# Performance work log

Hardware: AMD Instinct MI355X
Metric: run time of the kernel (lower is better)

The kernel has to match this reference:

```python
import jax, jax.numpy as jnp
import numpy as np

N_HEAD = 16
ROPE_BASE = 10000.0


def _rope(x):
    # x: (B, T, H, D), interleaved even/odd (GPT-NeoX style)
    B, T, H, D = x.shape
    inv_freq = 1.0 / (ROPE_BASE ** (jnp.arange(0, D, 2, dtype=jnp.float32) / D))
    t = jnp.arange(T, dtype=jnp.float32)
    freqs = t[:, None] * inv_freq[None, :]            # (T, D//2)
    cos = jnp.cos(freqs)[None, :, None, :]            # (1, T, 1, D//2)
    sin = jnp.sin(freqs)[None, :, None, :]
    x1, x2 = x[..., ::2], x[..., 1::2]
    y1 = x1 * cos - x2 * sin
    y2 = x1 * sin + x2 * cos
    return jnp.stack((y1, y2), axis=-1).reshape(B, T, H, D)


def setup_inputs() -> dict:
    key = jax.random.key(0)
    k1, k2, k3 = jax.random.split(key, 3)
    B, T, C = 4, 2048, 1024
    x = jax.random.normal(k1, (B, T, C), dtype=jnp.float32)
    W_attn = jax.random.normal(k2, (C, 3 * C), dtype=jnp.float32) * (1.0 / np.sqrt(C))
    W_proj = jax.random.normal(k3, (C, C), dtype=jnp.float32) * (1.0 / np.sqrt(C))
    return {"x": x, "W_attn": W_attn, "W_proj": W_proj}


def reference(x, W_attn, W_proj):
    B, T, C = x.shape
    H = N_HEAD
    D = C // H
    qkv = jnp.einsum('btc,cf->btf', x, W_attn)        # (B, T, 3C)
    q, k, v = jnp.split(qkv, 3, axis=-1)
    q = _rope(q.reshape(B, T, H, D))
    k = _rope(k.reshape(B, T, H, D))
    v = v.reshape(B, T, H, D)
    # (B, H, T, D)
    q = q.transpose(0, 2, 1, 3)
    k = k.transpose(0, 2, 1, 3)
    v = v.transpose(0, 2, 1, 3)
    scale = 1.0 / np.sqrt(D).astype(np.float32)
    scores = jnp.einsum('bhqd,bhkd->bhqk', q, k) * scale
    causal = jnp.tril(jnp.ones((T, T), dtype=bool))
    scores = jnp.where(causal[None, None], scores, jnp.finfo(scores.dtype).min)
    att = jax.nn.softmax(scores, axis=-1)
    y = jnp.einsum('bhqk,bhkd->bhqd', att, v)         # (B, H, T, D)
    y = y.transpose(0, 2, 1, 3).reshape(B, T, C)
    return jnp.einsum('btc,cf->btf', y, W_proj)
```

## Files before the change

kernel.cpp:

```cpp
#include <hip/hip_runtime.h>
#include <hip/hip_bf16.h>
#include <math.h>

typedef __attribute__((ext_vector_type(8))) __bf16 bf16x8;
typedef __attribute__((ext_vector_type(4))) float f32x4;
typedef __attribute__((ext_vector_type(16))) float f32x16;
typedef __attribute__((ext_vector_type(4))) unsigned short us4;

#define DEVINL static __device__ __forceinline__

DEVINL unsigned short f2bf(float f) {
  union { float f; unsigned int u; } v; v.f = f;
  return (unsigned short)((v.u + 0x7FFFu + ((v.u >> 16) & 1u)) >> 16);
}

DEVINL unsigned short f2bf_hw(float f) {
  __bf16 h = (__bf16)f;
  union { __bf16 h; unsigned short u; } v; v.h = h;
  return v.u;
}

DEVINL unsigned pk2(float a, float b) {
  return (unsigned)f2bf_hw(a) | ((unsigned)f2bf_hw(b) << 16);
}

DEVINL f32x4 mfma16(bf16x8 a, bf16x8 b, f32x4 c) {
  return __builtin_amdgcn_mfma_f32_16x16x32_bf16(a, b, c, 0, 0, 0);
}
DEVINL f32x16 mfma32(bf16x8 a, bf16x8 b, f32x16 c) {
  return __builtin_amdgcn_mfma_f32_32x32x16_bf16(a, b, c, 0, 0, 0);
}

#define GLOAD16(GP, LP)                                                        \
  __builtin_amdgcn_global_load_lds(                                            \
      (const __attribute__((address_space(1))) void*)(GP),                     \
      (__attribute__((address_space(3))) void*)(LP), 16, 0, 0)

static constexpr int kB = 4, kT = 2048, kC = 1024, kH = 16, kD = 64;
static constexpr int kM = kB * kT;

__global__ void cvt_x_kernel(const float* __restrict__ x,
                             unsigned short* __restrict__ xb, int n4) {
  int stride = gridDim.x * blockDim.x;
  for (int i = blockIdx.x * blockDim.x + threadIdx.x; i < n4; i += stride) {
    float4 v = ((const float4*)x)[i];
    us4 o;
    o[0] = f2bf(v.x); o[1] = f2bf(v.y); o[2] = f2bf(v.z); o[3] = f2bf(v.w);
    ((us4*)xb)[i] = o;
  }
}

__global__ void transpose_w_kernel(const float* __restrict__ W,
                                   unsigned short* __restrict__ WT,
                                   int K, int N) {
  __shared__ float tile[32][33];
  int n0 = blockIdx.x * 32, k0 = blockIdx.y * 32;
  int tx = threadIdx.x, ty = threadIdx.y;
#pragma unroll
  for (int i = 0; i < 4; ++i)
    tile[ty + i * 8][tx] = W[(size_t)(k0 + ty + i * 8) * N + n0 + tx];
  __syncthreads();
#pragma unroll
  for (int i = 0; i < 4; ++i)
    WT[(size_t)(n0 + ty + i * 8) * K + k0 + tx] = f2bf(tile[tx][ty + i * 8]);
}

__global__ void rope_table_kernel(float* __restrict__ cosT,
                                  float* __restrict__ sinT) {
  int idx = blockIdx.x * blockDim.x + threadIdx.x;
  if (idx >= kT * 32) return;
  int d2 = idx >> 11, t = idx & 2047;
  double ang = (double)t * pow(10000.0, -(double)d2 / 32.0);
  cosT[idx] = (float)cos(ang);
  sinT[idx] = (float)sin(ang);
}

template <int EPI>
__global__ __launch_bounds__(256) void gemm_bt_kernel(
    const unsigned short* __restrict__ A, const unsigned short* __restrict__ Bt,
    float* __restrict__ Cout, int Ndim, int Kdim,
    const float* __restrict__ cosT, const float* __restrict__ sinT,
    unsigned short* __restrict__ Qr, unsigned short* __restrict__ Kr,
    unsigned short* __restrict__ Vtg) {
  __shared__ unsigned short As[3][128 * 32];
  __shared__ unsigned short Bs[3][128 * 32];
  const int tid = threadIdx.x;
  const int wave = tid >> 6, lane = tid & 63;

  const int nwg = gridDim.x * gridDim.y;
  const int lin = blockIdx.y * gridDim.x + blockIdx.x;
  const int wg = (lin & 7) * (nwg >> 3) + (lin >> 3);
  const int n0 = (wg % gridDim.x) * 128, m0 = (wg / gridDim.x) * 128;

  const int wr = wave >> 1, wc = wave & 1;

  f32x4 acc[4][4] = {};

  const int srow = lane >> 2;
  const int scol = (((lane & 3) ^ ((lane >> 3) & 3)) << 3);
  const int fr = lane & 15;
  const int kswz = (((lane >> 4) ^ ((lane >> 1) & 3)) << 3);

  auto stage = [&](int k0, int bb) {
#pragma unroll
    for (int o = 0; o < 2; ++o) {
      int s = o * 4 + wave;
      int row = s * 16 + srow;
      GLOAD16(A + (size_t)(m0 + row) * Kdim + k0 + scol, &As[bb][s * 512]);
      GLOAD16(Bt + (size_t)(n0 + row) * Kdim + k0 + scol, &Bs[bb][s * 512]);
    }
  };

  const int NT = Kdim >> 5;
  stage(0, 0);
  stage(32, 1);

  for (int t = 0; t < NT; ++t) {
    const int buf = t % 3;
    if (t + 1 < NT) {
      asm volatile("s_waitcnt vmcnt(4)" ::: "memory");
    } else {
      asm volatile("s_waitcnt vmcnt(0)" ::: "memory");
    }
    __builtin_amdgcn_sched_barrier(0);
    __builtin_amdgcn_s_barrier();
    if (t + 2 < NT) stage((t + 2) << 5, (t + 2) % 3);

    bf16x8 af[4], bfr[4];
#pragma unroll
    for (int f = 0; f < 4; ++f)
      af[f] = *(const bf16x8*)&As[buf][(wr * 64 + f * 16 + fr) * 32 + kswz];
#pragma unroll
    for (int f = 0; f < 4; ++f)
      bfr[f] = *(const bf16x8*)&Bs[buf][(wc * 64 + f * 16 + fr) * 32 + kswz];
#pragma unroll
    for (int i = 0; i < 4; ++i)
#pragma unroll
      for (int j = 0; j < 4; ++j)
        acc[i][j] = mfma16(af[i], bfr[j], acc[i][j]);

    asm volatile("s_waitcnt lgkmcnt(0)" ::: "memory");
    __builtin_amdgcn_sched_barrier(0);
  }

  const int lr = (lane >> 4) * 4;
  const int fc = lane & 15;
  if (EPI == 0) {
#pragma unroll
    for (int i = 0; i < 4; ++i) {
      int mb = m0 + wr * 64 + i * 16 + lr;
#pragma unroll
      for (int j = 0; j < 4; ++j) {
        int n = n0 + wc * 64 + j * 16 + fc;
#pragma unroll
        for (int r = 0; r < 4; ++r)
          Cout[(size_t)(mb + r) * Ndim + n] = acc[i][j][r];
      }
    }
  } else {
#pragma unroll
    for (int i = 0; i < 4; ++i) {
      int mb = m0 + wr * 64 + i * 16 + lr;
      int b = mb >> 11, t0 = mb & 2047;
#pragma unroll
      for (int j = 0; j < 4; ++j) {
        int n = n0 + wc * 64 + j * 16 + fc;
        int sec = n >> 10;
        int c = n & 1023;
        int h = c >> 6, d = c & 63;
        size_t bh = (size_t)(b * 16 + h);
        if (sec == 2) {
          us4 pk;
#pragma unroll
          for (int r = 0; r < 4; ++r) pk[r] = f2bf(acc[i][j][r]);
          *(us4*)&Vtg[(bh * 64 + d) * 2048 + t0] = pk;
        } else {
          unsigned short* dst = (sec == 0) ? Qr : Kr;
          float4 c4 = *(const float4*)&cosT[(d >> 1) * 2048 + t0];
          float4 s4 = *(const float4*)&sinT[(d >> 1) * 2048 + t0];
          const float* cp = (const float*)&c4;
          const float* sp = (const float*)&s4;
#pragma unroll
          for (int r = 0; r < 4; ++r) {
            float v = acc[i][j][r];
            float pv = __shfl_xor(v, 1);
            float y = (d & 1) ? fmaf(pv, sp[r], v * cp[r])
                              : fmaf(v, cp[r], -pv * sp[r]);
            dst[(bh * 2048 + t0 + r) * 64 + d] = f2bf(y);
          }
        }
      }
    }
  }
}

__global__ __launch_bounds__(256, 2)
void attn_kernel(const unsigned short* __restrict__ Qr,
                 const unsigned short* __restrict__ Kr,
                 const unsigned short* __restrict__ Vtg,
                 unsigned short* __restrict__ Yb) {
  __shared__ unsigned short Ks[2][64 * 64];
  __shared__ unsigned short Vs[2][64 * 64];

  const int tid = threadIdx.x;
  const int wave = tid >> 6, lane = tid & 63;
  const int q31 = lane & 31, hi = lane >> 5;
  const int srow = lane >> 3;
  const int sblk = (lane & 7) ^ srow;
  const int rswz = (lane & 7) << 4;

  int lin = blockIdx.y * 8 + blockIdx.x;
  int wg = (lin & 7) * 64 + (lin >> 3);
  const int qpair = wg & 7;
  const int bh = wg >> 3;

  const unsigned short* Qg = Qr + (size_t)bh * 2048 * 64;
  const unsigned short* Kg = Kr + (size_t)bh * 2048 * 64;
  const unsigned short* Vg = Vtg + (size_t)bh * 64 * 2048;

  const float c = 0.18033688f;
  const float THR = 44.0f;

  auto stage = [&](int j, int bb) {
    int kv0s = j * 64;
#pragma unroll
    for (int o = 0; o < 2; ++o) {
      int s = o * 4 + wave;
      int row = s * 8 + srow;
      GLOAD16(Kg + ((size_t)(kv0s + row) * 64 + sblk * 8), &Ks[bb][s * 512]);
      GLOAD16(Vg + ((size_t)row * 2048 + kv0s + sblk * 8), &Vs[bb][s * 512]);
    }
  };

  for (int seg = 0; seg < 2; ++seg) {
    const int qblk = seg ? (15 - qpair) : qpair;
    const int q0 = qblk * 128;
    const int qw = q0 + wave * 32;
    const int qg = qw + q31;
    const int NT = 2 * qblk + 2;

    bf16x8 qf[4];
#pragma unroll
    for (int ds = 0; ds < 4; ++ds)
      qf[ds] = *(const bf16x8*)&Qg[(size_t)qg * 64 + ds * 16 + hi * 8];

    float mrow = -1e30f, lrow = 0.f;
    f32x16 y0 = {}, y1 = {};

    stage(0, 0);
    asm volatile("s_waitcnt vmcnt(0)" ::: "memory");
    __syncthreads();

    for (int t = 0; t < NT; ++t) {
      const int buf = t & 1;
      if (t + 1 < NT) stage(t + 1, buf ^ 1);
      const int kv0 = t * 64;

      if (kv0 <= qw + 31) {
        f32x16 st[2] = {};
        __builtin_amdgcn_s_setprio(1);
#pragma unroll
        for (int sub = 0; sub < 2; ++sub) {
          const unsigned char* kbase =
              (const unsigned char*)Ks[buf] + (sub * 32 + q31) * 128;
#pragma unroll
          for (int ds = 0; ds < 4; ++ds) {
            bf16x8 af = *(const bf16x8*)(kbase + ((ds * 32 + hi * 16) ^ rswz));
            st[sub] = mfma32(af, qf[ds], st[sub]);
          }
        }
        __builtin_amdgcn_s_setprio(0);

        if (kv0 + 63 > qw) {
#pragma unroll
          for (int sub = 0; sub < 2; ++sub)
#pragma unroll
            for (int r = 0; r < 16; ++r) {
              int kv = kv0 + sub * 32 + (r & 3) + 8 * (r >> 2) + 4 * hi;
              if (kv > qg) st[sub][r] = -1e30f;
            }
        }

        float tm = st[0][0];
#pragma unroll
        for (int r = 1; r < 16; ++r) tm = fmaxf(tm, st[0][r]);
#pragma unroll
        for (int r = 0; r < 16; ++r) tm = fmaxf(tm, st[1][r]);
        tm = fmaxf(tm, __shfl_xor(tm, 32));

        if (!__all(tm <= mrow + THR)) {
          float mn = fmaxf(mrow, tm);
          float al = __builtin_amdgcn_exp2f((mrow - mn) * c);
          mrow = mn;
          lrow *= al;
#pragma unroll
          for (int r = 0; r < 16; ++r) { y0[r] *= al; y1[r] *= al; }
        }

        const float mc = mrow * c;
        float ps = 0.f;
        unsigned pkw[2][8];
#pragma unroll
        for (int sub = 0; sub < 2; ++sub)
#pragma unroll
          for (int j = 0; j < 8; ++j) {
            float pa = __builtin_amdgcn_exp2f(fmaf(st[sub][2 * j], c, -mc));
            float pb = __builtin_amdgcn_exp2f(fmaf(st[sub][2 * j + 1], c, -mc));
            ps += pa + pb;
            pkw[sub][j] = pk2(pa, pb);
          }
        ps += __shfl_xor(ps, 32);
        lrow += ps;

        __builtin_amdgcn_s_setprio(1);
#pragma unroll
        for (int sub = 0; sub < 2; ++sub) {
#pragma unroll
          for (int ksl = 0; ksl < 2; ++ksl) {
            unsigned w0 = pkw[sub][ksl * 4 + 0], w2 = pkw[sub][ksl * 4 + 2];
            unsigned w1 = pkw[sub][ksl * 4 + 1], w3 = pkw[sub][ksl * 4 + 3];
            asm volatile("v_permlane32_swap_b32 %0, %1" : "+v"(w0), "+v"(w2));
            asm volatile("v_permlane32_swap_b32 %0, %1" : "+v"(w1), "+v"(w3));
            union { bf16x8 v; unsigned u[4]; } pf;
            pf.u[0] = w0; pf.u[1] = w1; pf.u[2] = w2; pf.u[3] = w3;
            const int cb = sub * 64 + ksl * 32 + hi * 16;
#pragma unroll
            for (int dm = 0; dm < 2; ++dm) {
              const int row = dm * 32 + q31;
              bf16x8 vf = *(const bf16x8*)((const unsigned char*)Vs[buf] +
                                           row * 128 + (cb ^ rswz));
              if (dm == 0) y0 = mfma32(vf, pf.v, y0);
              else         y1 = mfma32(vf, pf.v, y1);
            }
          }
        }
        __builtin_amdgcn_s_setprio(0);
      }

      __syncthreads();
    }

    const int b = bh >> 4, h = bh & 15;
    float inv = __builtin_amdgcn_rcpf(lrow);
    unsigned short* yrow = Yb + (size_t)(b * 2048 + qg) * 1024 + h * 64;
#pragma unroll
    for (int dm = 0; dm < 2; ++dm)
#pragma unroll
      for (int g = 0; g < 4; ++g) {
        us4 o;
#pragma unroll
        for (int e = 0; e < 4; ++e) {
          float yv = dm ? y1[g * 4 + e] : y0[g * 4 + e];
          o[e] = f2bf_hw(yv * inv);
        }
        *(us4*)&yrow[dm * 32 + g * 8 + hi * 4] = o;
      }
  }
}

extern "C" void kernel_launch(void* const* d_in, const int* in_sizes, int n_in,
                              void* d_out, int out_size, void* d_ws,
                              size_t ws_size, hipStream_t stream) {
  const float* x = (const float*)d_in[0];
  const float* Wa = (const float*)d_in[1];
  const float* Wp = (const float*)d_in[2];
  float* out = (float*)d_out;
  char* ws = (char*)d_ws;

  constexpr size_t OFF_WAT = 0;
  constexpr size_t OFF_WPT = 6291456;
  constexpr size_t OFF_COS = 8388608;
  constexpr size_t OFF_SIN = 8650752;
  constexpr size_t OFF_XB  = 8912896;
  constexpr size_t OFF_Q   = 25690112;
  constexpr size_t OFF_K   = 42467328;
  constexpr size_t OFF_V   = 59244544;

  unsigned short* WaT = (unsigned short*)(ws + OFF_WAT);
  unsigned short* WpT = (unsigned short*)(ws + OFF_WPT);
  float* cosT = (float*)(ws + OFF_COS);
  float* sinT = (float*)(ws + OFF_SIN);
  unsigned short* xb = (unsigned short*)(ws + OFF_XB);
  unsigned short* Yb = xb;
  unsigned short* Qr = (unsigned short*)(ws + OFF_Q);
  unsigned short* Kr = (unsigned short*)(ws + OFF_K);
  unsigned short* Vt = (unsigned short*)(ws + OFF_V);

  cvt_x_kernel<<<2048, 256, 0, stream>>>(x, xb, kM * kC / 4);
  transpose_w_kernel<<<dim3(96, 32), dim3(32, 8), 0, stream>>>(Wa, WaT, 1024, 3072);
  transpose_w_kernel<<<dim3(32, 32), dim3(32, 8), 0, stream>>>(Wp, WpT, 1024, 1024);
  rope_table_kernel<<<256, 256, 0, stream>>>(cosT, sinT);

  gemm_bt_kernel<1><<<dim3(24, 64), 256, 0, stream>>>(
      xb, WaT, nullptr, 3072, 1024, cosT, sinT, Qr, Kr, Vt);

  attn_kernel<<<dim3(8, 64), 256, 0, stream>>>(Qr, Kr, Vt, Yb);

  gemm_bt_kernel<0><<<dim3(8, 64), 256, 0, stream>>>(
      Yb, WpT, out, 1024, 1024, nullptr, nullptr, nullptr, nullptr, nullptr);
}
```

Measured before the change: 185.1 us.

## Enlarge GEMM tiles to 256x128x64 with 8 waves and split-phase pipelining

Reworks the bf16 MFMA GEMM to use 512-thread workgroups, each computing a 256x128 output tile with a K-step of 64. Global-to-LDS staging uses a new XOR swizzle and is split into two halves interleaved with two MFMA phases, which are wrapped in raised wave priority and barriers. The goal is more operand reuse per LDS byte and better overlap of loads with compute in both projection GEMMs. LDS use grows to about 144 KB and there are more barriers per iteration, which may limit occupancy. The epilogue row mapping depends on wr = wave>>1 now spanning four wave rows.

```diff
diff --git a/kernel.cpp b/kernel.cpp
--- a/kernel.cpp
+++ b/kernel.cpp
@@ -76,71 +76,114 @@
 }
 
 template <int EPI>
-__global__ __launch_bounds__(256) void gemm_bt_kernel(
+__global__ __launch_bounds__(512, 2) void gemm_bt_kernel(
     const unsigned short* __restrict__ A, const unsigned short* __restrict__ Bt,
     float* __restrict__ Cout, int Ndim, int Kdim,
     const float* __restrict__ cosT, const float* __restrict__ sinT,
     unsigned short* __restrict__ Qr, unsigned short* __restrict__ Kr,
     unsigned short* __restrict__ Vtg) {
-  __shared__ unsigned short As[3][128 * 32];
-  __shared__ unsigned short Bs[3][128 * 32];
+  __shared__ unsigned short As[3][256 * 64];
+  __shared__ unsigned short Bs[3][128 * 64];
   const int tid = threadIdx.x;
   const int wave = tid >> 6, lane = tid & 63;
 
   const int nwg = gridDim.x * gridDim.y;
   const int lin = blockIdx.y * gridDim.x + blockIdx.x;
   const int wg = (lin & 7) * (nwg >> 3) + (lin >> 3);
-  const int n0 = (wg % gridDim.x) * 128, m0 = (wg / gridDim.x) * 128;
+  const int n0 = (wg % gridDim.x) * 128, m0 = (wg / gridDim.x) * 256;
 
   const int wr = wave >> 1, wc = wave & 1;
 
   f32x4 acc[4][4] = {};
 
-  const int srow = lane >> 2;
-  const int scol = (((lane & 3) ^ ((lane >> 3) & 3)) << 3);
   const int fr = lane & 15;
-  const int kswz = (((lane >> 4) ^ ((lane >> 1) & 3)) << 3);
-
-  auto stage = [&](int k0, int bb) {
-#pragma unroll
-    for (int o = 0; o < 2; ++o) {
-      int s = o * 4 + wave;
-      int row = s * 16 + srow;
-      GLOAD16(A + (size_t)(m0 + row) * Kdim + k0 + scol, &As[bb][s * 512]);
-      GLOAD16(Bt + (size_t)(n0 + row) * Kdim + k0 + scol, &Bs[bb][s * 512]);
-    }
+
+  const int sblk = tid;
+  const int srow3 = sblk >> 3, skb = sblk & 7;
+  const int sgran = (skb ^ (srow3 & 7)) << 3;
+
+  auto stageA = [&](int t, int l) {
+    const int bb = t % 3;
+    const int k0 = t << 6;
+    const int row = (l << 6) + srow3;
+    GLOAD16(A + (size_t)(m0 + row) * Kdim + k0 + sgran,
+            &As[bb][(l * 512 + wave * 64) * 8]);
   };
-
-  const int NT = Kdim >> 5;
-  stage(0, 0);
-  stage(32, 1);
+  auto stageB = [&](int t, int l) {
+    const int bb = t % 3;
+    const int k0 = t << 6;
+    const int row = (l << 6) + srow3;
+    GLOAD16(Bt + (size_t)(n0 + row) * Kdim + k0 + sgran,
+            &Bs[bb][(l * 512 + wave * 64) * 8]);
+  };
+
+  const int NT = Kdim >> 6;
+
+  stageA(0, 0); stageA(0, 1); stageA(0, 2); stageA(0, 3);
+  stageB(0, 0); stageB(0, 1);
+  stageA(1, 0); stageA(1, 1); stageA(1, 2); stageA(1, 3);
+  stageB(1, 0); stageB(1, 1);
+  asm volatile("s_waitcnt vmcnt(6)" ::: "memory");
+  __builtin_amdgcn_sched_barrier(0);
+  __builtin_amdgcn_s_barrier();
+
+  const int rx = lane & 7, ku = lane >> 4;
 
   for (int t = 0; t < NT; ++t) {
     const int buf = t % 3;
-    if (t + 1 < NT) {
-      asm volatile("s_waitcnt vmcnt(4)" ::: "memory");
-    } else {
+    const unsigned char* Ab = (const unsigned char*)As[buf];
+    const unsigned char* Bb = (const unsigned char*)Bs[buf];
+    bf16x8 af[4], bfr[4];
+
+    {
+      const int col = ((ku ^ rx) << 4);
+#pragma unroll
+      for (int f = 0; f < 4; ++f)
+        af[f] = *(const bf16x8*)(Ab + (wr * 64 + f * 16 + fr) * 128 + col);
+#pragma unroll
+      for (int f = 0; f < 4; ++f)
+        bfr[f] = *(const bf16x8*)(Bb + (wc * 64 + f * 16 + fr) * 128 + col);
+    }
+    if (t + 2 < NT) { stageA(t + 2, 0); stageA(t + 2, 1); stageB(t + 2, 0); }
+    __builtin_amdgcn_s_barrier();
+    asm volatile("s_waitcnt lgkmcnt(0)" ::: "memory");
+    __builtin_amdgcn_sched_barrier(0);
+    __builtin_amdgcn_s_setprio(1);
+#pragma unroll
+    for (int i = 0; i < 4; ++i)
+#pragma unroll
+      for (int j = 0; j < 4; ++j)
+        acc[i][j] = mfma16(af[i], bfr[j], acc[i][j]);
+    __builtin_amdgcn_s_setprio(0);
+    __builtin_amdgcn_s_barrier();
+
+    {
+      const int col = (((4 | ku) ^ rx) << 4);
+#pragma unroll
+      for (int f = 0; f < 4; ++f)
+        af[f] = *(const bf16x8*)(Ab + (wr * 64 + f * 16 + fr) * 128 + col);
+#pragma unroll
+      for (int f = 0; f < 4; ++f)
+        bfr[f] = *(const bf16x8*)(Bb + (wc * 64 + f * 16 + fr) * 128 + col);
+    }
+    if (t + 2 < NT) { stageA(t + 2, 2); stageA(t + 2, 3); stageB(t + 2, 1); }
+    if (t + 2 < NT) {
+      asm volatile("s_waitcnt vmcnt(6)" ::: "memory");
+    } else if (t + 1 < NT) {
       asm volatile("s_waitcnt vmcnt(0)" ::: "memory");
     }
     __builtin_amdgcn_sched_barrier(0);
     __builtin_amdgcn_s_barrier();
-    if (t + 2 < NT) stage((t + 2) << 5, (t + 2) % 3);
-
-    bf16x8 af[4], bfr[4];
-#pragma unroll
-    for (int f = 0; f < 4; ++f)
-      af[f] = *(const bf16x8*)&As[buf][(wr * 64 + f * 16 + fr) * 32 + kswz];
-#pragma unroll
-    for (int f = 0; f < 4; ++f)
-      bfr[f] = *(const bf16x8*)&Bs[buf][(wc * 64 + f * 16 + fr) * 32 + kswz];
+    asm volatile("s_waitcnt lgkmcnt(0)" ::: "memory");
+    __builtin_amdgcn_sched_barrier(0);
+    __builtin_amdgcn_s_setprio(1);
 #pragma unroll
     for (int i = 0; i < 4; ++i)
 #pragma unroll
       for (int j = 0; j < 4; ++j)
         acc[i][j] = mfma16(af[i], bfr[j], acc[i][j]);
-
-    asm volatile("s_waitcnt lgkmcnt(0)" ::: "memory");
-    __builtin_amdgcn_sched_barrier(0);
+    __builtin_amdgcn_s_setprio(0);
+    __builtin_amdgcn_s_barrier();
   }
 
   const int lr = (lane >> 4) * 4;
@@ -391,11 +434,11 @@
   transpose_w_kernel<<<dim3(32, 32), dim3(32, 8), 0, stream>>>(Wp, WpT, 1024, 1024);
   rope_table_kernel<<<256, 256, 0, stream>>>(cosT, sinT);
 
-  gemm_bt_kernel<1><<<dim3(24, 64), 256, 0, stream>>>(
+  gemm_bt_kernel<1><<<dim3(24, 32), 512, 0, stream>>>(
       xb, WaT, nullptr, 3072, 1024, cosT, sinT, Qr, Kr, Vt);
 
   attn_kernel<<<dim3(8, 64), 256, 0, stream>>>(Qr, Kr, Vt, Yb);
 
-  gemm_bt_kernel<0><<<dim3(8, 64), 256, 0, stream>>>(
+  gemm_bt_kernel<0><<<dim3(8, 32), 512, 0, stream>>>(
       Yb, WpT, out, 1024, 1024, nullptr, nullptr, nullptr, nullptr, nullptr);
 }
```

New measurement: 182.1 us. Within noise of the previous version (-1.7%).
